# Optimization experiments

Hardware: AMD Instinct MI355X
Metric: run time of the kernel (lower is better)

## Reference

```python
import jax, jax.numpy as jnp
import numpy as np

B, C, D, H, W = 1, 32, 32, 128, 128


def setup_inputs() -> dict:
    key = jax.random.key(0)
    kx, kq, kk, kv, ko = jax.random.split(key, 5)
    s = 1.0 / np.sqrt(C)
    return {
        "x": jax.random.normal(kx, (B, C, D, H, W), dtype=jnp.float32),
        "Wq": jax.random.normal(kq, (C, C), dtype=jnp.float32) * s,
        "Wk": jax.random.normal(kk, (C, C), dtype=jnp.float32) * s,
        "Wv": jax.random.normal(kv, (C, C), dtype=jnp.float32) * s,
        "Wo": jax.random.normal(ko, (C, C), dtype=jnp.float32) * s,
    }


def reference(x, Wq, Wk, Wv, Wo):
    # x: [B, C, D, H, W]; multi-dimensional (axial) self-attention:
    # independent softmax-attention along each spatial axis, outputs summed.
    scale = jnp.asarray(x.shape[1], x.dtype) ** -0.5
    q = jnp.einsum("bcdhw,oc->bodhw", x, Wq)
    k = jnp.einsum("bcdhw,oc->bodhw", x, Wk)
    v = jnp.einsum("bcdhw,oc->bodhw", x, Wv)

    # attention along D axis: scores [B, H, W, D, D]
    ad = jax.nn.softmax(jnp.einsum("bcdhw,bcehw->bhwde", q, k) * scale, axis=-1)
    od = jnp.einsum("bhwde,bcehw->bcdhw", ad, v)

    # attention along H axis: scores [B, D, W, H, H]
    ah = jax.nn.softmax(jnp.einsum("bcdhw,bcdgw->bdwhg", q, k) * scale, axis=-1)
    oh = jnp.einsum("bdwhg,bcdgw->bcdhw", ah, v)

    # attention along W axis: scores [B, D, H, W, W]
    aw = jax.nn.softmax(jnp.einsum("bcdhw,bcdhu->bdhwu", q, k) * scale, axis=-1)
    ow = jnp.einsum("bdhwu,bcdhu->bcdhw", aw, v)

    out = jnp.einsum("bcdhw,oc->bodhw", od + oh + ow, Wo) + x  # residual
    return out
```

## Files before the change

kernel.cpp:

```cpp
#include <hip/hip_runtime.h>


#define C_ 32
#define D_ 32
#define H_ 128
#define W_ 128
#define SC (D_*H_*W_)
#define SD (H_*W_)
#define SH (W_)
#define SCALE 0.17677669529663687f

typedef __attribute__((ext_vector_type(8))) short short8;
typedef __attribute__((ext_vector_type(2))) short short2v;
typedef __attribute__((ext_vector_type(4))) float f32x4;

#define MFMA16(a,b,c) __builtin_amdgcn_mfma_f32_16x16x32_bf16(a,b,c,0,0,0)

__device__ __forceinline__ int xcd_swz(int bid, int nwg) {
    int chunk = nwg >> 3;
    return (bid & 7) * chunk + (bid >> 3);
}
__device__ __forceinline__ short bf16_trunc(float f) {
    return (short)(__float_as_uint(f) >> 16);
}
__device__ __forceinline__ short bf16_rtne(float f) {
    unsigned u = __float_as_uint(f);
    unsigned r = u + 0x7FFFu + ((u >> 16) & 1u);
    return (short)(r >> 16);
}
__device__ __forceinline__ float bf16_tof(short s) {
    return __uint_as_float(((unsigned)(unsigned short)s) << 16);
}

__device__ __forceinline__ void compute_M(const float* __restrict__ Wq,
                                          const float* __restrict__ Wk,
                                          float* Ms) {
    for (int o = threadIdx.x; o < 1024; o += 256) {
        int a = o >> 5, b = o & 31;
        float acc = 0.f;
        #pragma unroll
        for (int m = 0; m < 32; ++m) acc += Wq[m*32+a] * Wk[m*32+b];
        Ms[o] = acc * SCALE;
    }
}
__device__ __forceinline__ void compute_Mbf(const float* __restrict__ Wq,
                                            const float* __restrict__ Wk,
                                            short* Mh, short* Ml) {
    for (int o = threadIdx.x; o < 1024; o += 256) {
        int a = o >> 5, b = o & 31;
        float acc = 0.f;
        #pragma unroll
        for (int m = 0; m < 32; ++m) acc += Wq[m*32+a] * Wk[m*32+b];
        acc *= SCALE;
        short h = bf16_trunc(acc);
        Mh[o] = h;
        Ml[o] = bf16_trunc(acc - bf16_tof(h));
    }
}

#define TT_STRIDE 40
#define XH_STRIDE 136
#define P_STRIDE  136
#define R_BYTES   36864

__device__ __forceinline__ void slice_engine(
        const float* Xf, const short* Mh, const short* Ml,
        short* Tt_h, short* Tt_l, short* P, short* Xh,
        f32x4 uacc[2][2])
{
    const int t = threadIdx.x;
    const int wv = t >> 6, l = t & 63, hi = l >> 4, r = l & 15;
    const int qb = wv * 32;

    #pragma unroll
    for (int k = 0; k < 8; ++k) {
        int idx = t + k*256;
        int u2 = idx & 63, c = idx >> 6;
        float2 v = *(const float2*)&Xf[c*128 + u2*2];
        short2v h; h[0] = bf16_rtne(v.x); h[1] = bf16_rtne(v.y);
        *(short2v*)&Xh[c*XH_STRIDE + u2*2] = h;
    }

    short8 xh_[2], xl_[2];
    #pragma unroll
    for (int nt = 0; nt < 2; ++nt) {
        int u = qb + nt*16 + r;
        #pragma unroll
        for (int j = 0; j < 8; ++j) {
            float f = Xf[(hi*8 + j)*128 + u];
            short h = bf16_trunc(f);
            xh_[nt][j] = h; xl_[nt][j] = bf16_trunc(f - bf16_tof(h));
        }
    }

    short8 mah[2], mal[2];
    #pragma unroll
    for (int mt = 0; mt < 2; ++mt) {
        mah[mt] = *(const short8*)&Mh[(r + 16*mt)*32 + hi*8];
        mal[mt] = *(const short8*)&Ml[(r + 16*mt)*32 + hi*8];
    }
    f32x4 tacc[2][2] = {};
    #pragma unroll
    for (int nt = 0; nt < 2; ++nt) {
        #pragma unroll
        for (int mt = 0; mt < 2; ++mt) {
            tacc[mt][nt] = MFMA16(mah[mt], xh_[nt], tacc[mt][nt]);
            tacc[mt][nt] = MFMA16(mah[mt], xl_[nt], tacc[mt][nt]);
            tacc[mt][nt] = MFMA16(mal[mt], xh_[nt], tacc[mt][nt]);
        }
    }
    #pragma unroll
    for (int mt = 0; mt < 2; ++mt)
    #pragma unroll
    for (int nt = 0; nt < 2; ++nt) {
        int u = qb + nt*16 + r;
        #pragma unroll
        for (int rp = 0; rp < 2; ++rp) {
            int c0 = 16*mt + 4*hi + 2*rp;
            float f0 = tacc[mt][nt][2*rp], f1 = tacc[mt][nt][2*rp+1];
            short h0 = bf16_trunc(f0), h1 = bf16_trunc(f1);
            short2v vh; vh[0] = h0; vh[1] = h1;
            *(short2v*)&Tt_h[u*TT_STRIDE + c0] = vh;
            short2v vl; vl[0] = bf16_trunc(f0 - bf16_tof(h0));
            vl[1] = bf16_trunc(f1 - bf16_tof(h1));
            *(short2v*)&Tt_l[u*TT_STRIDE + c0] = vl;
        }
    }
    __syncthreads();

    f32x4 sacc[2][8] = {};
    #pragma unroll
    for (int nt = 0; nt < 8; ++nt) {
        short8 th = *(const short8*)&Tt_h[(nt*16 + r)*TT_STRIDE + hi*8];
        short8 tl = *(const short8*)&Tt_l[(nt*16 + r)*TT_STRIDE + hi*8];
        #pragma unroll
        for (int qt = 0; qt < 2; ++qt) {
            sacc[qt][nt] = MFMA16(xh_[qt], th, sacc[qt][nt]);
            sacc[qt][nt] = MFMA16(xh_[qt], tl, sacc[qt][nt]);
            sacc[qt][nt] = MFMA16(xl_[qt], th, sacc[qt][nt]);
        }
    }
    float rls[2][4];
    #pragma unroll
    for (int qt = 0; qt < 2; ++qt)
    #pragma unroll
    for (int reg = 0; reg < 4; ++reg) {
        float m = sacc[qt][0][reg];
        #pragma unroll
        for (int nt = 1; nt < 8; ++nt) m = fmaxf(m, sacc[qt][nt][reg]);
        m = fmaxf(m, __shfl_xor(m, 1));
        m = fmaxf(m, __shfl_xor(m, 2));
        m = fmaxf(m, __shfl_xor(m, 4));
        m = fmaxf(m, __shfl_xor(m, 8));
        float s = 0.f;
        #pragma unroll
        for (int nt = 0; nt < 8; ++nt) {
            float e = __expf(sacc[qt][nt][reg] - m);
            sacc[qt][nt][reg] = e; s += e;
        }
        s += __shfl_xor(s, 1);
        s += __shfl_xor(s, 2);
        s += __shfl_xor(s, 4);
        s += __shfl_xor(s, 8);
        rls[qt][reg] = 1.f / s;
    }
    __syncthreads();
    #pragma unroll
    for (int qt = 0; qt < 2; ++qt)
    #pragma unroll
    for (int reg = 0; reg < 4; ++reg) {
        int q = qb + 16*qt + 4*hi + reg;
        float rl = rls[qt][reg];
        #pragma unroll
        for (int nt = 0; nt < 8; ++nt)
            P[q*P_STRIDE + nt*16 + r] = bf16_rtne(sacc[qt][nt][reg] * rl);
    }
    __syncthreads();

    #pragma unroll
    for (int kt = 0; kt < 4; ++kt) {
        short8 xa[2], pb[2];
        #pragma unroll
        for (int mt = 0; mt < 2; ++mt)
            xa[mt] = *(const short8*)&Xh[(r + 16*mt)*XH_STRIDE + hi*8 + kt*32];
        #pragma unroll
        for (int nt = 0; nt < 2; ++nt)
            pb[nt] = *(const short8*)&P[(qb + 16*nt + r)*P_STRIDE + hi*8 + kt*32];
        #pragma unroll
        for (int mt = 0; mt < 2; ++mt)
        #pragma unroll
        for (int nt = 0; nt < 2; ++nt)
            uacc[mt][nt] = MFMA16(xa[mt], pb[nt], uacc[mt][nt]);
    }
}

__global__ __launch_bounds__(256) void kw_kernel(const float* __restrict__ x,
        const float* __restrict__ Wq, const float* __restrict__ Wk,
        float* __restrict__ U) {
    __shared__ __align__(16) char Rr[R_BYTES];
    __shared__ __align__(16) short Xh[32*XH_STRIDE];
    __shared__ __align__(16) short MhS[1024], MlS[1024];
    float* Xf = (float*)Rr;
    short* Tt_h = (short*)(Rr + 16384);
    short* Tt_l = (short*)(Rr + 26624);
    short* P = (short*)Rr;
    int bid = xcd_swz(blockIdx.x, gridDim.x);
    int d = bid >> 7, h = bid & 127;
    int t = threadIdx.x;
    compute_Mbf(Wq, Wk, MhS, MlS);
    const float* xs = x + d*SD + h*SH;
    #pragma unroll
    for (int k = 0; k < 4; ++k) {
        int idx = t + k*256;
        int c = idx >> 5, u4 = idx & 31;
        *(float4*)&Xf[c*128 + u4*4] = *(const float4*)&xs[c*SC + u4*4];
    }
    __syncthreads();
    f32x4 uacc[2][2] = {};
    slice_engine(Xf, MhS, MlS, Tt_h, Tt_l, P, Xh, uacc);
    const int wv = t >> 6, l = t & 63, hi = l >> 4, r = l & 15;
    float* Uo = U + d*SD + h*SH;
    #pragma unroll
    for (int mt = 0; mt < 2; ++mt)
    #pragma unroll
    for (int nt = 0; nt < 2; ++nt)
    #pragma unroll
    for (int reg = 0; reg < 4; ++reg) {
        int c = 16*mt + 4*hi + reg;
        int q = wv*32 + 16*nt + r;
        Uo[c*SC + q] = uacc[mt][nt][reg];
    }
}

__global__ __launch_bounds__(256) void kh_kernel(const float* __restrict__ x,
        const float* __restrict__ Wq, const float* __restrict__ Wk,
        float* __restrict__ U) {
    __shared__ __align__(16) char Rr[R_BYTES];
    __shared__ __align__(16) float Xf1[32*128];
    __shared__ __align__(16) short Xh[32*XH_STRIDE];
    __shared__ __align__(16) short MhS[1024], MlS[1024];
    float* Xf0 = (float*)Rr;
    short* Tt_h = (short*)(Rr + 16384);
    short* Tt_l = (short*)(Rr + 26624);
    short* P = (short*)Rr;
    int bid = xcd_swz(blockIdx.x, gridDim.x);
    int d = bid >> 6, w0 = (bid & 63) * 2;
    int t = threadIdx.x;
    compute_Mbf(Wq, Wk, MhS, MlS);
    const float* xs = x + d*SD + w0;
    #pragma unroll
    for (int k = 0; k < 16; ++k) {
        int idx = t + k*256;
        int c = idx >> 7, g = idx & 127;
        float2 v = *(const float2*)&xs[c*SC + g*SH];
        Xf0[c*128+g] = v.x;
        Xf1[c*128+g] = v.y;
    }
    __syncthreads();
    f32x4 u0[2][2] = {}, u1[2][2] = {};
    slice_engine(Xf0, MhS, MlS, Tt_h, Tt_l, P, Xh, u0);
    __syncthreads();
    slice_engine(Xf1, MhS, MlS, Tt_h, Tt_l, P, Xh, u1);
    const int wv = t >> 6, l = t & 63, hi = l >> 4, r = l & 15;
    float* Uo = U + d*SD + w0;
    #pragma unroll
    for (int mt = 0; mt < 2; ++mt)
    #pragma unroll
    for (int nt = 0; nt < 2; ++nt)
    #pragma unroll
    for (int reg = 0; reg < 4; ++reg) {
        int c = 16*mt + 4*hi + reg;
        int q = wv*32 + 16*nt + r;
        float2* p = (float2*)&Uo[c*SC + q*SH];
        float2 v = *p;
        v.x += u0[mt][nt][reg];
        v.y += u1[mt][nt][reg];
        *p = v;
    }
}

#define PD 1032
__global__ __launch_bounds__(256) void kd_kernel(const float* __restrict__ x,
        const float* __restrict__ Wq, const float* __restrict__ Wk,
        const float* __restrict__ Wv, const float* __restrict__ Wo,
        float* UO) {
    __shared__ float Xs[8*PD];
    __shared__ float Ts[8*PD];
    __shared__ float Ms[1024];
    __shared__ float Ps[32*33];
    int bid = xcd_swz(blockIdx.x, gridDim.x);
    int h = bid >> 4, w0 = (bid & 15) * 8;
    int t = threadIdx.x;
    compute_M(Wq, Wk, Ms);
    for (int o = t; o < 1024; o += 256) {
        int oo = o >> 5, c = o & 31;
        float acc = 0.f;
        #pragma unroll
        for (int m = 0; m < 32; ++m) acc += Wo[oo*32+m] * Wv[m*32+c];
        Ps[oo*33+c] = acc;
    }
    const float* xs = x + h*SH + w0;
    for (int o = t; o < 2048; o += 256) {
        int j4 = o & 1, dd = (o >> 1) & 31, c = o >> 6;
        float4 v = *reinterpret_cast<const float4*>(xs + c*SC + dd*SD + j4*4);
        int base = c*32 + dd;
        Xs[(j4*4+0)*PD + base] = v.x;
        Xs[(j4*4+1)*PD + base] = v.y;
        Xs[(j4*4+2)*PD + base] = v.z;
        Xs[(j4*4+3)*PD + base] = v.w;
    }
    __syncthreads();
    for (int o = t; o < 8192; o += 256) {
        int j = o >> 10, rr = o & 1023, c = rr >> 5, e = rr & 31;
        float acc = 0.f;
        #pragma unroll
        for (int c2 = 0; c2 < 32; ++c2) acc += Ms[c*32+c2] * Xs[j*PD + c2*32 + e];
        Ts[j*PD + c*32 + e] = acc;
    }
    __syncthreads();
    int j = t & 7, q = t >> 3;
    float s[32];
    #pragma unroll
    for (int e = 0; e < 32; ++e) s[e] = 0.f;
    for (int c = 0; c < 32; ++c) {
        float xc = Xs[j*PD + c*32 + q];
        const float4* tr = reinterpret_cast<const float4*>(&Ts[j*PD + c*32]);
        #pragma unroll
        for (int e4 = 0; e4 < 8; ++e4) {
            float4 tv = tr[e4];
            s[e4*4+0] += xc*tv.x; s[e4*4+1] += xc*tv.y;
            s[e4*4+2] += xc*tv.z; s[e4*4+3] += xc*tv.w;
        }
    }
    float m = -1e30f;
    #pragma unroll
    for (int e = 0; e < 32; ++e) m = fmaxf(m, s[e]);
    float l = 0.f;
    #pragma unroll
    for (int e = 0; e < 32; ++e) { float ee = __expf(s[e]-m); s[e] = ee; l += ee; }
    float rl = 1.f / l;
    int site = q*SD + h*SH + w0 + j;
    float u[32];
    for (int c = 0; c < 32; ++c) {
        const float4* xr = reinterpret_cast<const float4*>(&Xs[j*PD + c*32]);
        float acc = 0.f;
        #pragma unroll
        for (int e4 = 0; e4 < 8; ++e4) {
            float4 xv = xr[e4];
            acc += s[e4*4+0]*xv.x + s[e4*4+1]*xv.y
                 + s[e4*4+2]*xv.z + s[e4*4+3]*xv.w;
        }
        u[c] = UO[site + c*SC] + acc * rl;
    }
    #pragma unroll
    for (int o = 0; o < 32; ++o) {
        float acc = x[site + o*SC];
        #pragma unroll
        for (int c = 0; c < 32; ++c) acc += Ps[o*33+c] * u[c];
        UO[site + o*SC] = acc;
    }
}

extern "C" void kernel_launch(void* const* d_in, const int* in_sizes, int n_in,
                              void* d_out, int out_size, void* d_ws, size_t ws_size,
                              hipStream_t stream) {
    (void)in_sizes; (void)n_in; (void)out_size; (void)d_ws; (void)ws_size;
    const float* x  = (const float*)d_in[0];
    const float* Wq = (const float*)d_in[1];
    const float* Wk = (const float*)d_in[2];
    const float* Wv = (const float*)d_in[3];
    const float* Wo = (const float*)d_in[4];
    float* U = (float*)d_out;
    kw_kernel<<<dim3(4096), dim3(256), 0, stream>>>(x, Wq, Wk, U);
    kh_kernel<<<dim3(2048), dim3(256), 0, stream>>>(x, Wq, Wk, U);
    kd_kernel<<<dim3(2048), dim3(256), 0, stream>>>(x, Wq, Wk, Wv, Wo, U);
}
```

Baseline: 431.6 us.

## Port D-axis attention kernel to bf16 split-precision MFMA with LDS-staged epilogue

Rewrites kd_kernel so the M·X, score, P·V and output-projection matmuls run on bf16 MFMA 16x16x32 instructions instead of scalar FP32 FMAs. Precision is kept by splitting operands into hi/lo bf16 pairs and issuing three MFMAs per product. The running U accumulator is prefetched from global memory during the first pass, staged in LDS and then re-tiled for the final projection. It also asks for two blocks per CU through launch bounds. The cost is more LDS traffic and slightly lower precision for the probability tensor, which is rounded to a single bf16.

```diff
diff --git a/kernel.cpp b/kernel.cpp
--- a/kernel.cpp
+++ b/kernel.cpp
@@ -11,6 +11,7 @@
 #define SCALE 0.17677669529663687f
 
 typedef __attribute__((ext_vector_type(8))) short short8;
+typedef __attribute__((ext_vector_type(4))) short short4v;
 typedef __attribute__((ext_vector_type(2))) short short2v;
 typedef __attribute__((ext_vector_type(4))) float f32x4;
 
@@ -31,18 +32,15 @@
 __device__ __forceinline__ float bf16_tof(short s) {
     return __uint_as_float(((unsigned)(unsigned short)s) << 16);
 }
-
-__device__ __forceinline__ void compute_M(const float* __restrict__ Wq,
-                                          const float* __restrict__ Wk,
-                                          float* Ms) {
-    for (int o = threadIdx.x; o < 1024; o += 256) {
-        int a = o >> 5, b = o & 31;
-        float acc = 0.f;
-        #pragma unroll
-        for (int m = 0; m < 32; ++m) acc += Wq[m*32+a] * Wk[m*32+b];
-        Ms[o] = acc * SCALE;
-    }
-}
+__device__ __forceinline__ short8 ld8_b64x2(const short* p) {
+    short4v a = *(const short4v*)p;
+    short4v b = *(const short4v*)(p + 4);
+    short8 o;
+    o[0]=a[0]; o[1]=a[1]; o[2]=a[2]; o[3]=a[3];
+    o[4]=b[0]; o[5]=b[1]; o[6]=b[2]; o[7]=b[3];
+    return o;
+}
+
 __device__ __forceinline__ void compute_Mbf(const float* __restrict__ Wq,
                                             const float* __restrict__ Wk,
                                             short* Mh, short* Ml) {
@@ -55,6 +53,19 @@
         short h = bf16_trunc(acc);
         Mh[o] = h;
         Ml[o] = bf16_trunc(acc - bf16_tof(h));
+    }
+}
+__device__ __forceinline__ void compute_Pbf(const float* __restrict__ Wv,
+                                            const float* __restrict__ Wo,
+                                            short* Ph, short* Pl) {
+    for (int o = threadIdx.x; o < 1024; o += 256) {
+        int oo = o >> 5, c = o & 31;
+        float acc = 0.f;
+        #pragma unroll
+        for (int m = 0; m < 32; ++m) acc += Wo[oo*32+m] * Wv[m*32+c];
+        short h = bf16_trunc(acc);
+        Ph[o] = h;
+        Pl[o] = bf16_trunc(acc - bf16_tof(h));
     }
 }
 
@@ -279,85 +290,197 @@
     }
 }
 
-#define PD 1032
-__global__ __launch_bounds__(256) void kd_kernel(const float* __restrict__ x,
+#define XJ 1152
+#define KD_TTS 40
+#define KD_PS  36
+__global__ __launch_bounds__(256, 2) void kd_kernel(const float* __restrict__ x,
         const float* __restrict__ Wq, const float* __restrict__ Wk,
         const float* __restrict__ Wv, const float* __restrict__ Wo,
-        float* UO) {
-    __shared__ float Xs[8*PD];
-    __shared__ float Ts[8*PD];
-    __shared__ float Ms[1024];
-    __shared__ float Ps[32*33];
+        float* __restrict__ UO) {
+    __shared__ __align__(16) short Mh[1024], Ml[1024], Psh[1024], Psl[1024];
+    __shared__ __align__(16) short Xh[8*XJ], Xl[8*XJ];
+    __shared__ __align__(16) char Rr[33792];
+    short* Tt_h = (short*)Rr;
+    short* Tt_l = (short*)(Rr + 10240);
+    short* Pp   = (short*)(Rr + 20480);
+    float* u_lds = (float*)Rr;
+
     int bid = xcd_swz(blockIdx.x, gridDim.x);
     int h = bid >> 4, w0 = (bid & 15) * 8;
     int t = threadIdx.x;
-    compute_M(Wq, Wk, Ms);
-    for (int o = t; o < 1024; o += 256) {
-        int oo = o >> 5, c = o & 31;
-        float acc = 0.f;
-        #pragma unroll
-        for (int m = 0; m < 32; ++m) acc += Wo[oo*32+m] * Wv[m*32+c];
-        Ps[oo*33+c] = acc;
-    }
+    const int wv = t >> 6, l = t & 63, hi = l >> 4, r = l & 15;
+
+    compute_Mbf(Wq, Wk, Mh, Ml);
+    compute_Pbf(Wv, Wo, Psh, Psl);
+
     const float* xs = x + h*SH + w0;
-    for (int o = t; o < 2048; o += 256) {
-        int j4 = o & 1, dd = (o >> 1) & 31, c = o >> 6;
-        float4 v = *reinterpret_cast<const float4*>(xs + c*SC + dd*SD + j4*4);
-        int base = c*32 + dd;
-        Xs[(j4*4+0)*PD + base] = v.x;
-        Xs[(j4*4+1)*PD + base] = v.y;
-        Xs[(j4*4+2)*PD + base] = v.z;
-        Xs[(j4*4+3)*PD + base] = v.w;
-    }
-    __syncthreads();
-    for (int o = t; o < 8192; o += 256) {
-        int j = o >> 10, rr = o & 1023, c = rr >> 5, e = rr & 31;
-        float acc = 0.f;
-        #pragma unroll
-        for (int c2 = 0; c2 < 32; ++c2) acc += Ms[c*32+c2] * Xs[j*PD + c2*32 + e];
-        Ts[j*PD + c*32 + e] = acc;
-    }
-    __syncthreads();
-    int j = t & 7, q = t >> 3;
-    float s[32];
-    #pragma unroll
-    for (int e = 0; e < 32; ++e) s[e] = 0.f;
-    for (int c = 0; c < 32; ++c) {
-        float xc = Xs[j*PD + c*32 + q];
-        const float4* tr = reinterpret_cast<const float4*>(&Ts[j*PD + c*32]);
-        #pragma unroll
-        for (int e4 = 0; e4 < 8; ++e4) {
-            float4 tv = tr[e4];
-            s[e4*4+0] += xc*tv.x; s[e4*4+1] += xc*tv.y;
-            s[e4*4+2] += xc*tv.z; s[e4*4+3] += xc*tv.w;
-        }
-    }
-    float m = -1e30f;
-    #pragma unroll
-    for (int e = 0; e < 32; ++e) m = fmaxf(m, s[e]);
-    float l = 0.f;
-    #pragma unroll
-    for (int e = 0; e < 32; ++e) { float ee = __expf(s[e]-m); s[e] = ee; l += ee; }
-    float rl = 1.f / l;
-    int site = q*SD + h*SH + w0 + j;
-    float u[32];
-    for (int c = 0; c < 32; ++c) {
-        const float4* xr = reinterpret_cast<const float4*>(&Xs[j*PD + c*32]);
-        float acc = 0.f;
-        #pragma unroll
-        for (int e4 = 0; e4 < 8; ++e4) {
-            float4 xv = xr[e4];
-            acc += s[e4*4+0]*xv.x + s[e4*4+1]*xv.y
-                 + s[e4*4+2]*xv.z + s[e4*4+3]*xv.w;
-        }
-        u[c] = UO[site + c*SC] + acc * rl;
-    }
-    #pragma unroll
-    for (int o = 0; o < 32; ++o) {
-        float acc = x[site + o*SC];
-        #pragma unroll
-        for (int c = 0; c < 32; ++c) acc += Ps[o*33+c] * u[c];
-        UO[site + o*SC] = acc;
+    #pragma unroll
+    for (int k = 0; k < 8; ++k) {
+        int o = t + k*256;
+        int j4 = o & 1, d = (o >> 1) & 31, c = o >> 6;
+        float4 v = *(const float4*)(xs + c*SC + d*SD + j4*4);
+        float fr[4] = {v.x, v.y, v.z, v.w};
+        #pragma unroll
+        for (int i = 0; i < 4; ++i) {
+            short hh = bf16_trunc(fr[i]);
+            Xh[((j4*4+i)*32 + c)*KD_PS + d] = hh;
+            Xl[((j4*4+i)*32 + c)*KD_PS + d] = bf16_trunc(fr[i] - bf16_tof(hh));
+        }
+    }
+    __syncthreads();
+
+    short8 mah[2], mal[2], pah[2], pal[2];
+    #pragma unroll
+    for (int mt = 0; mt < 2; ++mt) {
+        mah[mt] = *(const short8*)&Mh[(mt*16 + r)*32 + hi*8];
+        mal[mt] = *(const short8*)&Ml[(mt*16 + r)*32 + hi*8];
+        pah[mt] = *(const short8*)&Psh[(mt*16 + r)*32 + hi*8];
+        pal[mt] = *(const short8*)&Psl[(mt*16 + r)*32 + hi*8];
+    }
+
+    f32x4 uacc[2][2][2] = {};
+    float4 upre[8];
+
+    #pragma unroll
+    for (int ps = 0; ps < 2; ++ps) {
+        int j = ps*4 + wv;
+        const short* Xhj = &Xh[j*XJ];
+        const short* Xlj = &Xl[j*XJ];
+        short8 xph[2], xpl[2];
+        #pragma unroll
+        for (int et = 0; et < 2; ++et)
+        #pragma unroll
+        for (int jj = 0; jj < 8; ++jj) {
+            int c = hi*8 + jj;
+            xph[et][jj] = Xhj[c*KD_PS + et*16 + r];
+            xpl[et][jj] = Xlj[c*KD_PS + et*16 + r];
+        }
+        f32x4 tacc[2][2] = {};
+        #pragma unroll
+        for (int et = 0; et < 2; ++et)
+        #pragma unroll
+        for (int mt = 0; mt < 2; ++mt) {
+            tacc[mt][et] = MFMA16(mah[mt], xph[et], tacc[mt][et]);
+            tacc[mt][et] = MFMA16(mah[mt], xpl[et], tacc[mt][et]);
+            tacc[mt][et] = MFMA16(mal[mt], xph[et], tacc[mt][et]);
+        }
+        int tb = wv*32*KD_TTS;
+        #pragma unroll
+        for (int mt = 0; mt < 2; ++mt)
+        #pragma unroll
+        for (int et = 0; et < 2; ++et) {
+            int e = et*16 + r;
+            #pragma unroll
+            for (int rp = 0; rp < 2; ++rp) {
+                int c0 = mt*16 + hi*4 + rp*2;
+                float f0 = tacc[mt][et][rp*2], f1 = tacc[mt][et][rp*2+1];
+                short h0 = bf16_trunc(f0), h1 = bf16_trunc(f1);
+                short2v vh; vh[0] = h0; vh[1] = h1;
+                *(short2v*)&Tt_h[tb + e*KD_TTS + c0] = vh;
+                short2v vl; vl[0] = bf16_trunc(f0 - bf16_tof(h0));
+                vl[1] = bf16_trunc(f1 - bf16_tof(h1));
+                *(short2v*)&Tt_l[tb + e*KD_TTS + c0] = vl;
+            }
+        }
+        f32x4 sacc[2][2] = {};
+        #pragma unroll
+        for (int et = 0; et < 2; ++et) {
+            short8 th = *(const short8*)&Tt_h[tb + (et*16 + r)*KD_TTS + hi*8];
+            short8 tl = *(const short8*)&Tt_l[tb + (et*16 + r)*KD_TTS + hi*8];
+            #pragma unroll
+            for (int qt = 0; qt < 2; ++qt) {
+                sacc[qt][et] = MFMA16(xph[qt], th, sacc[qt][et]);
+                sacc[qt][et] = MFMA16(xph[qt], tl, sacc[qt][et]);
+                sacc[qt][et] = MFMA16(xpl[qt], th, sacc[qt][et]);
+            }
+        }
+        int pb = wv*32*KD_PS;
+        #pragma unroll
+        for (int qt = 0; qt < 2; ++qt)
+        #pragma unroll
+        for (int reg = 0; reg < 4; ++reg) {
+            float m = fmaxf(sacc[qt][0][reg], sacc[qt][1][reg]);
+            m = fmaxf(m, __shfl_xor(m, 1));
+            m = fmaxf(m, __shfl_xor(m, 2));
+            m = fmaxf(m, __shfl_xor(m, 4));
+            m = fmaxf(m, __shfl_xor(m, 8));
+            float e0 = __expf(sacc[qt][0][reg] - m);
+            float e1 = __expf(sacc[qt][1][reg] - m);
+            float s = e0 + e1;
+            s += __shfl_xor(s, 1);
+            s += __shfl_xor(s, 2);
+            s += __shfl_xor(s, 4);
+            s += __shfl_xor(s, 8);
+            float rl = 1.f / s;
+            int d = qt*16 + hi*4 + reg;
+            Pp[pb + d*KD_PS + 0*16 + r] = bf16_rtne(e0 * rl);
+            Pp[pb + d*KD_PS + 1*16 + r] = bf16_rtne(e1 * rl);
+        }
+        #pragma unroll
+        for (int mt = 0; mt < 2; ++mt) {
+            short8 xa = ld8_b64x2(&Xhj[(mt*16 + r)*KD_PS + hi*8]);
+            #pragma unroll
+            for (int nt = 0; nt < 2; ++nt) {
+                short8 pbf = ld8_b64x2(&Pp[pb + (nt*16 + r)*KD_PS + hi*8]);
+                uacc[ps][mt][nt] = MFMA16(xa, pbf, uacc[ps][mt][nt]);
+            }
+        }
+        if (ps == 0) {
+            #pragma unroll
+            for (int k = 0; k < 8; ++k) {
+                int o = t + k*256;
+                int j4 = o & 1, d = (o >> 1) & 31, c = o >> 6;
+                upre[k] = *(const float4*)(UO + c*SC + d*SD + h*SH + w0 + j4*4);
+            }
+        }
+    }
+    __syncthreads();
+    #pragma unroll
+    for (int k = 0; k < 8; ++k) {
+        int o = t + k*256;
+        int j4 = o & 1, d = (o >> 1) & 31, c = o >> 6;
+        *(float4*)&u_lds[c*264 + d*8 + j4*4] = upre[k];
+    }
+    __syncthreads();
+    #pragma unroll
+    for (int ps = 0; ps < 2; ++ps)
+    #pragma unroll
+    for (int mt = 0; mt < 2; ++mt)
+    #pragma unroll
+    for (int nt = 0; nt < 2; ++nt)
+    #pragma unroll
+    for (int reg = 0; reg < 4; ++reg) {
+        int c = mt*16 + hi*4 + reg;
+        u_lds[c*264 + (nt*16 + r)*8 + ps*4 + wv] += uacc[ps][mt][nt][reg];
+    }
+    __syncthreads();
+    f32x4 eacc[2][4] = {};
+    #pragma unroll
+    for (int nt = 0; nt < 4; ++nt) {
+        short8 bh, bl;
+        #pragma unroll
+        for (int jj = 0; jj < 8; ++jj) {
+            float f = u_lds[(hi*8 + jj)*264 + wv*64 + nt*16 + r];
+            short hh = bf16_trunc(f);
+            bh[jj] = hh; bl[jj] = bf16_trunc(f - bf16_tof(hh));
+        }
+        #pragma unroll
+        for (int mt = 0; mt < 2; ++mt) {
+            eacc[mt][nt] = MFMA16(pah[mt], bh, eacc[mt][nt]);
+            eacc[mt][nt] = MFMA16(pah[mt], bl, eacc[mt][nt]);
+            eacc[mt][nt] = MFMA16(pal[mt], bh, eacc[mt][nt]);
+        }
+    }
+    #pragma unroll
+    for (int mt = 0; mt < 2; ++mt)
+    #pragma unroll
+    for (int nt = 0; nt < 4; ++nt)
+    #pragma unroll
+    for (int reg = 0; reg < 4; ++reg) {
+        int o = mt*16 + hi*4 + reg;
+        int s = wv*64 + nt*16 + r;
+        int addr = o*SC + (s >> 3)*SD + h*SH + w0 + (s & 7);
+        UO[addr] = eacc[mt][nt][reg] + x[addr];
     }
 }
 
```

Result: faster. 379.5 us (-12.1%).
